# Kernel tuning notes

Hardware: AMD Instinct MI355X
Metric: run time of the kernel (lower is better)

## Reference

```python
import jax, jax.numpy as jnp
import numpy as np

B, L, D, H, DH = 2, 2048, 1024, 16, 64
EPS = 1e-5
ROPE_BASE = 10000.0


def _layernorm(x, w, b):
    mu = jnp.mean(x, axis=-1, keepdims=True)
    var = jnp.var(x, axis=-1, keepdims=True)
    y = (x - mu) * jax.lax.rsqrt(var + EPS)
    y = y * w
    if b is not None:
        y = y + b
    return y


def _rope(x):
    # x: [B, L, H, DH]; GPT-NeoX-style rotation over the full head dim
    inv_freq = 1.0 / (ROPE_BASE ** (jnp.arange(0, DH, 2, dtype=jnp.float32) / DH))  # [DH/2]
    t = jnp.arange(L, dtype=jnp.float32)
    freqs = jnp.outer(t, inv_freq)                       # [L, DH/2]
    cos = jnp.concatenate([jnp.cos(freqs)] * 2, axis=-1)[:, None, :]  # [L, 1, DH]
    sin = jnp.concatenate([jnp.sin(freqs)] * 2, axis=-1)[:, None, :]
    x1, x2 = jnp.split(x, 2, axis=-1)
    rot = jnp.concatenate([-x2, x1], axis=-1)
    return x * cos + rot * sin


def setup_inputs() -> dict:
    key = jax.random.key(0)
    ks = jax.random.split(key, 3)
    x = jax.random.normal(ks[0], (B, L, D), dtype=jnp.float32)
    w_qkv = jax.random.normal(ks[1], (3 * D, D), dtype=jnp.float32) * (D ** -0.5)
    w_out = jax.random.normal(ks[2], (D, D), dtype=jnp.float32) * (D ** -0.5)
    return {
        "x": x,
        "ln_w": jnp.ones((D,), jnp.float32),
        "ln_b": jnp.zeros((D,), jnp.float32),
        "w_qkv": w_qkv,
        "q_ln_w": jnp.ones((D,), jnp.float32),
        "k_ln_w": jnp.ones((D,), jnp.float32),
        "w_out": w_out,
    }


def reference(x, ln_w, ln_b, w_qkv, q_ln_w, k_ln_w, w_out):
    h = _layernorm(x, ln_w, ln_b)                         # [B, L, D]
    qkv = jnp.einsum("bld,ed->ble", h, w_qkv)            # [B, L, 3D]
    q, k, v = jnp.split(qkv, 3, axis=-1)
    q = _layernorm(q, q_ln_w, None)                       # weight-only per-token LN
    k = _layernorm(k, k_ln_w, None)
    q = _rope(q.reshape(B, L, H, DH))                     # [B, L, H, DH]
    k = _rope(k.reshape(B, L, H, DH))
    v = v.reshape(B, L, H, DH)
    ctx = jax.nn.dot_product_attention(q, k, v)           # [B, L, H, DH], scale 1/sqrt(DH)
    ctx = ctx.reshape(B, L, D)
    return jnp.einsum("bld,od->blo", ctx, w_out)
```

## Files before the change

kernel.cpp:

```cpp
#include <hip/hip_runtime.h>
#include <math.h>

#define BB 2
#define LL 2048
#define DD 1024
#define HH 16
#define DHD 64
#define NT (BB*LL)
#define D3 (3*DD)
#define D2 (2*DD)

typedef __bf16 bf16x8 __attribute__((ext_vector_type(8)));
typedef float  f32x4  __attribute__((ext_vector_type(4)));

__device__ __forceinline__ f32x4 mfma16(bf16x8 a, bf16x8 b, f32x4 c) {
    return __builtin_amdgcn_mfma_f32_16x16x32_bf16(a, b, c, 0, 0, 0);
}

__device__ __forceinline__ unsigned short f2bf(float f) {
    unsigned int u = __float_as_uint(f);
    u = (u + 0x7FFFu + ((u >> 16) & 1u)) >> 16;
    return (unsigned short)u;
}
__device__ __forceinline__ float bf2f(unsigned short s) {
    return __uint_as_float(((unsigned int)s) << 16);
}

__device__ __forceinline__ void gload16(const void* g, void* l) {
    __builtin_amdgcn_global_load_lds(
        (const __attribute__((address_space(1))) void*)g,
        (__attribute__((address_space(3))) void*)l, 16, 0, 0);
}

__device__ __forceinline__ float wred(float v) {
#pragma unroll
    for (int off = 32; off > 0; off >>= 1) v += __shfl_down(v, off, 64);
    return v;
}

__device__ __forceinline__ unsigned int pack_bf2(float p0, float p1) {
    const unsigned int u0 = __float_as_uint(p0) + 0x8000u;
    const unsigned int u1 = __float_as_uint(p1) + 0x8000u;
    return __builtin_amdgcn_perm(u1, u0, 0x07060302u);
}

__global__ __launch_bounds__(256) void ln_cvt_kernel(
        const float* __restrict__ x, const float* __restrict__ w,
        const float* __restrict__ b, unsigned short* __restrict__ h,
        const float* __restrict__ wq, unsigned short* __restrict__ wqb,
        const float* __restrict__ wo, unsigned short* __restrict__ wob) {
    const int bx = blockIdx.x;
    const int tid = threadIdx.x;
    if (bx >= NT) {
        int i = (bx - NT) * 256 + tid;
        const float* s; unsigned short* d;
        if (i < 786432) { s = wq; d = wqb; }
        else            { i -= 786432; s = wo; d = wob; }
        const float4 v = ((const float4*)s)[i];
        ((ushort4*)d)[i] = make_ushort4(f2bf(v.x), f2bf(v.y), f2bf(v.z), f2bf(v.w));
        return;
    }
    const float4 v = ((const float4*)(x + (size_t)bx * DD))[tid];
    float s = v.x + v.y + v.z + v.w;
    float ss = v.x*v.x + v.y*v.y + v.z*v.z + v.w*v.w;
    s = wred(s); ss = wred(ss);
    __shared__ float red[8];
    if ((tid & 63) == 0) { red[tid >> 6] = s; red[4 + (tid >> 6)] = ss; }
    __syncthreads();
    s  = red[0] + red[1] + red[2] + red[3];
    ss = red[4] + red[5] + red[6] + red[7];
    const float mu  = s * (1.0f / DD);
    const float inv = rsqrtf(ss * (1.0f / DD) - mu * mu + 1e-5f);
    const float4 wv = ((const float4*)w)[tid];
    const float4 bv = ((const float4*)b)[tid];
    *(ushort4*)(h + (size_t)bx * DD + tid * 4) = make_ushort4(
        f2bf((v.x - mu) * inv * wv.x + bv.x),
        f2bf((v.y - mu) * inv * wv.y + bv.y),
        f2bf((v.z - mu) * inv * wv.z + bv.z),
        f2bf((v.w - mu) * inv * wv.w + bv.w));
}

__global__ __launch_bounds__(256) void gemm_qkv(
        const unsigned short* __restrict__ A, const unsigned short* __restrict__ B,
        unsigned short* __restrict__ qk, unsigned short* __restrict__ vt) {
    const int K = DD;
    __shared__ unsigned short As[128 * 32];
    __shared__ unsigned short Bs[128 * 32];
    const int tid = threadIdx.x;
    const int w = tid >> 6, lane = tid & 63;
    const int l15 = lane & 15, quad = lane >> 4;
    const int wr = w >> 1, wc = w & 1;
    const int m0 = blockIdx.y << 7, n0 = blockIdx.x << 7;

    const int srow = w * 32 + (lane >> 2);
    const int skel = (lane & 3) << 3;
    const unsigned short* gA = A + (size_t)(m0 + srow) * K + skel;
    const unsigned short* gB = B + (size_t)(n0 + srow) * K + skel;
    unsigned short* lA = &As[w * 1024];
    unsigned short* lB = &Bs[w * 1024];

    f32x4 acc[4][4];
#pragma unroll
    for (int i = 0; i < 4; i++)
#pragma unroll
        for (int j = 0; j < 4; j++) acc[i][j] = (f32x4){0.f, 0.f, 0.f, 0.f};

    for (int k0 = 0; k0 < K; k0 += 32) {
        gload16(gA + k0,                 lA);
        gload16(gA + k0 + (size_t)16*K,  lA + 512);
        gload16(gB + k0,                 lB);
        gload16(gB + k0 + (size_t)16*K,  lB + 512);
        __syncthreads();
        bf16x8 af[4], bg[4];
#pragma unroll
        for (int i = 0; i < 4; i++) {
            af[i] = *(const bf16x8*)&As[(wr*64 + i*16 + l15) * 32 + quad*8];
            bg[i] = *(const bf16x8*)&Bs[(wc*64 + i*16 + l15) * 32 + quad*8];
        }
#pragma unroll
        for (int i = 0; i < 4; i++)
#pragma unroll
            for (int j = 0; j < 4; j++)
                acc[i][j] = mfma16(af[i], bg[j], acc[i][j]);
        __syncthreads();
    }
    if (n0 < D2) {
#pragma unroll
        for (int i = 0; i < 4; i++) {
            const int mrow = m0 + wr*64 + i*16 + quad*4;
#pragma unroll
            for (int j = 0; j < 4; j++) {
                const int ncol = n0 + wc*64 + j*16 + l15;
#pragma unroll
                for (int r = 0; r < 4; r++)
                    qk[(size_t)(mrow + r) * D2 + ncol] = f2bf(acc[i][j][r]);
            }
        }
    } else {
#pragma unroll
        for (int i = 0; i < 4; i++) {
            const int mrow = m0 + wr*64 + i*16 + quad*4;
            const int bb = mrow >> 11, l = mrow & (LL - 1);
#pragma unroll
            for (int j = 0; j < 4; j++) {
                const int nv = n0 + wc*64 + j*16 + l15 - D2;
                const int hh = nv >> 6, dh = nv & 63;
                *(ushort4*)&vt[((size_t)(bb*HH + hh) * DHD + dh) * LL + l] =
                    make_ushort4(f2bf(acc[i][j][0]), f2bf(acc[i][j][1]),
                                 f2bf(acc[i][j][2]), f2bf(acc[i][j][3]));
            }
        }
    }
}

__global__ __launch_bounds__(256) void gemm_out(
        const unsigned short* __restrict__ A, const unsigned short* __restrict__ B,
        float* __restrict__ C, int M, int N, int K) {
    __shared__ unsigned short As[128 * 32];
    __shared__ unsigned short Bs[128 * 32];
    const int tid = threadIdx.x;
    const int w = tid >> 6, lane = tid & 63;
    const int l15 = lane & 15, quad = lane >> 4;
    const int wr = w >> 1, wc = w & 1;
    const int m0 = blockIdx.y << 7, n0 = blockIdx.x << 7;
    const int srow = w * 32 + (lane >> 2);
    const int skel = (lane & 3) << 3;
    const unsigned short* gA = A + (size_t)(m0 + srow) * K + skel;
    const unsigned short* gB = B + (size_t)(n0 + srow) * K + skel;
    unsigned short* lA = &As[w * 1024];
    unsigned short* lB = &Bs[w * 1024];
    f32x4 acc[4][4];
#pragma unroll
    for (int i = 0; i < 4; i++)
#pragma unroll
        for (int j = 0; j < 4; j++) acc[i][j] = (f32x4){0.f, 0.f, 0.f, 0.f};
    for (int k0 = 0; k0 < K; k0 += 32) {
        gload16(gA + k0,                 lA);
        gload16(gA + k0 + (size_t)16*K,  lA + 512);
        gload16(gB + k0,                 lB);
        gload16(gB + k0 + (size_t)16*K,  lB + 512);
        __syncthreads();
        bf16x8 af[4], bg[4];
#pragma unroll
        for (int i = 0; i < 4; i++) {
            af[i] = *(const bf16x8*)&As[(wr*64 + i*16 + l15) * 32 + quad*8];
            bg[i] = *(const bf16x8*)&Bs[(wc*64 + i*16 + l15) * 32 + quad*8];
        }
#pragma unroll
        for (int i = 0; i < 4; i++)
#pragma unroll
            for (int j = 0; j < 4; j++)
                acc[i][j] = mfma16(af[i], bg[j], acc[i][j]);
        __syncthreads();
    }
#pragma unroll
    for (int i = 0; i < 4; i++) {
        const int mrow = m0 + wr*64 + i*16 + quad*4;
#pragma unroll
        for (int j = 0; j < 4; j++) {
            const int ncol = n0 + wc*64 + j*16 + l15;
#pragma unroll
            for (int r = 0; r < 4; r++)
                C[(size_t)(mrow + r) * N + ncol] = acc[i][j][r];
        }
    }
}

__global__ __launch_bounds__(256) void qk_rope_kernel(
        const unsigned short* __restrict__ qk,
        const float* __restrict__ qw, const float* __restrict__ kw,
        unsigned short* __restrict__ qarr, unsigned short* __restrict__ karr) {
    const int t = blockIdx.x;
    const int l = t & (LL - 1), b = t >> 11;
    const int tid = threadIdx.x;
    const unsigned short* base = qk + (size_t)t * D2;
    const ushort4 qu = *(const ushort4*)(base + tid * 4);
    const ushort4 ku = *(const ushort4*)(base + DD + tid * 4);
    const float q[4] = {bf2f(qu.x), bf2f(qu.y), bf2f(qu.z), bf2f(qu.w)};
    const float k[4] = {bf2f(ku.x), bf2f(ku.y), bf2f(ku.z), bf2f(ku.w)};
    float sq = q[0]+q[1]+q[2]+q[3], ssq = q[0]*q[0]+q[1]*q[1]+q[2]*q[2]+q[3]*q[3];
    float sk = k[0]+k[1]+k[2]+k[3], ssk = k[0]*k[0]+k[1]*k[1]+k[2]*k[2]+k[3]*k[3];
    sq = wred(sq); ssq = wred(ssq); sk = wred(sk); ssk = wred(ssk);
    __shared__ float red[16];
    __shared__ float qs[DD], ks[DD];
    const int wid = tid >> 6;
    if ((tid & 63) == 0) { red[wid] = sq; red[4+wid] = ssq; red[8+wid] = sk; red[12+wid] = ssk; }
    __syncthreads();
    sq = red[0]+red[1]+red[2]+red[3];    ssq = red[4]+red[5]+red[6]+red[7];
    sk = red[8]+red[9]+red[10]+red[11];  ssk = red[12]+red[13]+red[14]+red[15];
    const float muq = sq * (1.f/DD), invq = rsqrtf(ssq*(1.f/DD) - muq*muq + 1e-5f);
    const float muk = sk * (1.f/DD), invk = rsqrtf(ssk*(1.f/DD) - muk*muk + 1e-5f);
    const float4 qwv = ((const float4*)qw)[tid];
    const float4 kwv = ((const float4*)kw)[tid];
    const float qwa[4] = {qwv.x, qwv.y, qwv.z, qwv.w};
    const float kwa[4] = {kwv.x, kwv.y, kwv.z, kwv.w};
    float qn[4], kn[4];
#pragma unroll
    for (int e = 0; e < 4; e++) {
        qn[e] = (q[e] - muq) * invq * qwa[e];
        kn[e] = (k[e] - muk) * invk * kwa[e];
    }
    *(float4*)&qs[tid*4] = make_float4(qn[0], qn[1], qn[2], qn[3]);
    *(float4*)&ks[tid*4] = make_float4(kn[0], kn[1], kn[2], kn[3]);
    __syncthreads();
    const int d = tid * 4, j0 = d & 63;
    const bool first = (j0 < 32);
    const int pt = first ? (tid + 8) : (tid - 8);
    const float4 qp4 = *(const float4*)&qs[pt*4];
    const float4 kp4 = *(const float4*)&ks[pt*4];
    const float qb[4] = {qp4.x, qp4.y, qp4.z, qp4.w};
    const float kb[4] = {kp4.x, kp4.y, kp4.z, kp4.w};
    const float lf = (float)l;
    const float QS = 0.125f * 1.44269504088896340736f;
    unsigned short oq[4], ok[4];
#pragma unroll
    for (int e = 0; e < 4; e++) {
        const float fi   = (float)((j0 & 31) + e);
        const float freq = expf(fi * (-0.28782313662425576f));
        const float ang  = lf * freq;
        const float c = cosf(ang), sn = sinf(ang);
        float vq, vk;
        if (first) { vq = qn[e]*c - qb[e]*sn; vk = kn[e]*c - kb[e]*sn; }
        else       { vq = qn[e]*c + qb[e]*sn; vk = kn[e]*c + kb[e]*sn; }
        oq[e] = f2bf(vq * QS);
        ok[e] = f2bf(vk);
    }
    const int hh = tid >> 4;
    const int dh = (tid * 4) & 63;
    const size_t ro = ((size_t)(b*HH + hh) * LL + l) * DHD + dh;
    *(ushort4*)(qarr + ro) = make_ushort4(oq[0], oq[1], oq[2], oq[3]);
    *(ushort4*)(karr + ro) = make_ushort4(ok[0], ok[1], ok[2], ok[3]);
}

__global__ __launch_bounds__(256, 4) void attn_kernel(
        const unsigned short* __restrict__ qarr,
        const unsigned short* __restrict__ karr,
        const unsigned short* __restrict__ vt,
        unsigned short* __restrict__ opart,
        float* __restrict__ lpart) {
    const int x = blockIdx.x;
    const int g  = (x & 7) | ((x >> 7) << 3);
    const int qblk = (x >> 3) & 15;
    const int s = g & 1, bh = g >> 1;
    const int b = bh >> 4, h = bh & 15;
    const int q0 = qblk << 7;
    const int kvbase = s << 10;
    const int tid = threadIdx.x, w = tid >> 6, lane = tid & 63;
    const int l15 = lane & 15, quad = lane >> 4;

    __shared__ unsigned short Ks[64 * 64];
    __shared__ unsigned short Vs[64 * 64];
    __shared__ unsigned short Pw[4][2][16][72];

    const unsigned short* kbase = karr + ((size_t)bh * LL + kvbase) * DHD;
    const unsigned short* vbase = vt   + (size_t)bh * DHD * LL + kvbase;

    bf16x8 qf[2][2];
    {
        const unsigned short* qp = qarr + ((size_t)bh*LL + q0 + w*32 + l15) * DHD + quad*8;
#pragma unroll
        for (int qt = 0; qt < 2; qt++)
#pragma unroll
            for (int c = 0; c < 2; c++)
                qf[qt][c] = *(const bf16x8*)(qp + qt*16*DHD + c*32);
    }

    bf16x8 ones;
#pragma unroll
    for (int i = 0; i < 8; i++) ones[i] = (__bf16)1.0f;

    const int r8 = lane >> 3, sc = lane & 7;
    f32x4 o[2][4], lacc[2];
#pragma unroll
    for (int qt = 0; qt < 2; qt++) {
        lacc[qt] = (f32x4){0.f, 0.f, 0.f, 0.f};
#pragma unroll
        for (int nt = 0; nt < 4; nt++) o[qt][nt] = (f32x4){0.f, 0.f, 0.f, 0.f};
    }

#pragma unroll
    for (int rd = 0; rd < 2; rd++) {
        const int row = w*8 + rd*32 + r8;
        const int chunk = sc ^ (row & 7);
        gload16(kbase + (size_t)row * DHD + chunk*8, (char*)Ks + w*1024 + rd*4096);
        gload16(vbase + (size_t)row * LL + chunk*8,  (char*)Vs + w*1024 + rd*4096);
    }

    for (int kt = 0; kt < 16; kt++) {
        __syncthreads();
        bf16x8 kf[4][2], vf[4][2];
#pragma unroll
        for (int t = 0; t < 4; t++)
#pragma unroll
            for (int c = 0; c < 2; c++) {
                const int slot = (quad + c*4) ^ (l15 & 7);
                kf[t][c] = *(const bf16x8*)&Ks[(t*16 + l15) * DHD + slot*8];
                vf[t][c] = *(const bf16x8*)&Vs[(t*16 + l15) * DHD + slot*8];
            }
        __syncthreads();
        if (kt + 1 < 16) {
#pragma unroll
            for (int rd = 0; rd < 2; rd++) {
                const int row = w*8 + rd*32 + r8;
                const int chunk = sc ^ (row & 7);
                gload16(kbase + ((size_t)((kt+1)*64 + row)) * DHD + chunk*8,
                        (char*)Ks + w*1024 + rd*4096);
                gload16(vbase + (size_t)row * LL + (kt+1)*64 + chunk*8,
                        (char*)Vs + w*1024 + rd*4096);
            }
        }

#pragma unroll
        for (int qt = 0; qt < 2; qt++) {
            f32x4 st[4];
#pragma unroll
            for (int t = 0; t < 4; t++) {
                f32x4 z = (f32x4){-64.f, -64.f, -64.f, -64.f};
                z = mfma16(kf[t][0], qf[qt][0], z);
                z = mfma16(kf[t][1], qf[qt][1], z);
                st[t] = z;
            }
#pragma unroll
            for (int t = 0; t < 4; t++) {
                const float p0 = __builtin_amdgcn_exp2f(st[t][0]);
                const float p1 = __builtin_amdgcn_exp2f(st[t][1]);
                const float p2 = __builtin_amdgcn_exp2f(st[t][2]);
                const float p3 = __builtin_amdgcn_exp2f(st[t][3]);
                uint2 pk;
                pk.x = pack_bf2(p0, p1);
                pk.y = pack_bf2(p2, p3);
                *(uint2*)&Pw[w][qt][l15][t*16 + quad*4] = pk;
            }
            const bf16x8 ap0 = *(const bf16x8*)&Pw[w][qt][l15][quad*8];
            const bf16x8 ap1 = *(const bf16x8*)&Pw[w][qt][l15][32 + quad*8];
            lacc[qt] = mfma16(ap0, ones, lacc[qt]);
            lacc[qt] = mfma16(ap1, ones, lacc[qt]);
#pragma unroll
            for (int nt = 0; nt < 4; nt++) {
                f32x4 t0 = o[qt][nt];
                t0 = mfma16(ap0, vf[nt][0], t0);
                t0 = mfma16(ap1, vf[nt][1], t0);
                o[qt][nt] = t0;
            }
        }
    }

    unsigned short* op = opart + (size_t)s * NT * DD;
#pragma unroll
    for (int qt = 0; qt < 2; qt++) {
#pragma unroll
        for (int r = 0; r < 4; r++) {
            const int qrow = q0 + w*32 + qt*16 + quad*4 + r;
            const size_t token = (size_t)b * LL + qrow;
#pragma unroll
            for (int nt = 0; nt < 4; nt++)
                op[token * DD + h*DHD + nt*16 + l15] = f2bf(o[qt][nt][r]);
        }
        if (l15 == 0) {
#pragma unroll
            for (int r = 0; r < 4; r++)
                lpart[((size_t)s * BB*HH + bh) * LL + q0 + w*32 + qt*16 + quad*4 + r] =
                    lacc[qt][r];
        }
    }
}

__global__ __launch_bounds__(256) void combine_kernel(
        const unsigned short* __restrict__ opart, const float* __restrict__ lpart,
        unsigned short* __restrict__ ctx) {
    const int token = blockIdx.x;
    const int tid = threadIdx.x;
    const int b = token >> 11, l = token & (LL - 1);
    const int h = tid >> 4;
    const size_t idx = (size_t)token * DD + tid * 4;
    const ushort4 a = *(const ushort4*)(opart + idx);
    const ushort4 c = *(const ushort4*)(opart + (size_t)NT * DD + idx);
    const float l1 = lpart[((size_t)(b*HH + h)) * LL + l];
    const float l2 = lpart[((size_t)BB*HH*LL) + ((size_t)(b*HH + h)) * LL + l];
    const float inv = 1.0f / (l1 + l2);
    *(ushort4*)(ctx + idx) = make_ushort4(
        f2bf((bf2f(a.x) + bf2f(c.x)) * inv),
        f2bf((bf2f(a.y) + bf2f(c.y)) * inv),
        f2bf((bf2f(a.z) + bf2f(c.z)) * inv),
        f2bf((bf2f(a.w) + bf2f(c.w)) * inv));
}

extern "C" void kernel_launch(void* const* d_in, const int* in_sizes, int n_in,
                              void* d_out, int out_size, void* d_ws, size_t ws_size,
                              hipStream_t stream) {
    const float* x      = (const float*)d_in[0];
    const float* ln_w   = (const float*)d_in[1];
    const float* ln_b   = (const float*)d_in[2];
    const float* w_qkv  = (const float*)d_in[3];
    const float* q_ln_w = (const float*)d_in[4];
    const float* k_ln_w = (const float*)d_in[5];
    const float* w_out  = (const float*)d_in[6];
    float* out = (float*)d_out;

    char* ws = (char*)d_ws;
    unsigned short* hb    = (unsigned short*)ws;
    unsigned short* karr  = (unsigned short*)ws;
    unsigned short* ctxb  = (unsigned short*)ws;
    unsigned short* qk    = (unsigned short*)(ws + ((size_t)8  << 20));
    unsigned short* opart = (unsigned short*)(ws + ((size_t)8  << 20));
    unsigned short* vtp   = (unsigned short*)(ws + ((size_t)24 << 20));
    unsigned short* qarr  = (unsigned short*)(ws + ((size_t)32 << 20));
    unsigned short* wqb   = (unsigned short*)(ws + ((size_t)40 << 20));
    float*          lpart = (float*)(ws + ((size_t)40 << 20));
    unsigned short* wob   = (unsigned short*)(ws + ((size_t)46 << 20));

    ln_cvt_kernel<<<NT + 4096, 256, 0, stream>>>(x, ln_w, ln_b, hb,
                                                 w_qkv, wqb, w_out, wob);
    gemm_qkv<<<dim3(D3/128, NT/128), 256, 0, stream>>>(hb, wqb, qk, vtp);
    qk_rope_kernel<<<NT, 256, 0, stream>>>(qk, q_ln_w, k_ln_w, qarr, karr);
    attn_kernel<<<1024, 256, 0, stream>>>(qarr, karr, vtp, opart, lpart);
    combine_kernel<<<NT, 256, 0, stream>>>(opart, lpart, ctxb);
    gemm_out<<<dim3(DD/128, NT/128), 256, 0, stream>>>(ctxb, wob, out, NT, DD, DD);
}
```

Baseline: 245.8 us.

## Split attention KV into four chunks and halve output GEMM row tile

```diff
diff --git a/kernel.cpp b/kernel.cpp
--- a/kernel.cpp
+++ b/kernel.cpp
@@ -9,6 +9,8 @@
 #define NT (BB*LL)
 #define D3 (3*DD)
 #define D2 (2*DD)
+#define NSPLIT 4
+#define KVCH (LL/NSPLIT)
 
 typedef __bf16 bf16x8 __attribute__((ext_vector_type(8)));
 typedef float  f32x4  __attribute__((ext_vector_type(4)));
@@ -156,46 +158,45 @@
 __global__ __launch_bounds__(256) void gemm_out(
         const unsigned short* __restrict__ A, const unsigned short* __restrict__ B,
         float* __restrict__ C, int M, int N, int K) {
-    __shared__ unsigned short As[128 * 32];
+    __shared__ unsigned short As[64 * 32];
     __shared__ unsigned short Bs[128 * 32];
     const int tid = threadIdx.x;
     const int w = tid >> 6, lane = tid & 63;
     const int l15 = lane & 15, quad = lane >> 4;
     const int wr = w >> 1, wc = w & 1;
-    const int m0 = blockIdx.y << 7, n0 = blockIdx.x << 7;
-    const int srow = w * 32 + (lane >> 2);
+    const int m0 = blockIdx.y << 6, n0 = blockIdx.x << 7;
     const int skel = (lane & 3) << 3;
-    const unsigned short* gA = A + (size_t)(m0 + srow) * K + skel;
-    const unsigned short* gB = B + (size_t)(n0 + srow) * K + skel;
-    unsigned short* lA = &As[w * 1024];
+    const unsigned short* gA = A + (size_t)(m0 + w*16 + (lane >> 2)) * K + skel;
+    const unsigned short* gB = B + (size_t)(n0 + w*32 + (lane >> 2)) * K + skel;
+    unsigned short* lA = &As[w * 512];
     unsigned short* lB = &Bs[w * 1024];
-    f32x4 acc[4][4];
-#pragma unroll
-    for (int i = 0; i < 4; i++)
+    f32x4 acc[2][4];
+#pragma unroll
+    for (int i = 0; i < 2; i++)
 #pragma unroll
         for (int j = 0; j < 4; j++) acc[i][j] = (f32x4){0.f, 0.f, 0.f, 0.f};
     for (int k0 = 0; k0 < K; k0 += 32) {
         gload16(gA + k0,                 lA);
-        gload16(gA + k0 + (size_t)16*K,  lA + 512);
         gload16(gB + k0,                 lB);
         gload16(gB + k0 + (size_t)16*K,  lB + 512);
         __syncthreads();
-        bf16x8 af[4], bg[4];
-#pragma unroll
-        for (int i = 0; i < 4; i++) {
-            af[i] = *(const bf16x8*)&As[(wr*64 + i*16 + l15) * 32 + quad*8];
-            bg[i] = *(const bf16x8*)&Bs[(wc*64 + i*16 + l15) * 32 + quad*8];
-        }
-#pragma unroll
-        for (int i = 0; i < 4; i++)
+        bf16x8 af[2], bg[4];
+#pragma unroll
+        for (int i = 0; i < 2; i++)
+            af[i] = *(const bf16x8*)&As[(wr*32 + i*16 + l15) * 32 + quad*8];
+#pragma unroll
+        for (int j = 0; j < 4; j++)
+            bg[j] = *(const bf16x8*)&Bs[(wc*64 + j*16 + l15) * 32 + quad*8];
+#pragma unroll
+        for (int i = 0; i < 2; i++)
 #pragma unroll
             for (int j = 0; j < 4; j++)
                 acc[i][j] = mfma16(af[i], bg[j], acc[i][j]);
         __syncthreads();
     }
 #pragma unroll
-    for (int i = 0; i < 4; i++) {
-        const int mrow = m0 + wr*64 + i*16 + quad*4;
+    for (int i = 0; i < 2; i++) {
+        const int mrow = m0 + wr*32 + i*16 + quad*4;
 #pragma unroll
         for (int j = 0; j < 4; j++) {
             const int ncol = n0 + wc*64 + j*16 + l15;
@@ -276,21 +277,22 @@
         const unsigned short* __restrict__ qarr,
         const unsigned short* __restrict__ karr,
         const unsigned short* __restrict__ vt,
-        unsigned short* __restrict__ opart,
+        unsigned short* __restrict__ op0, unsigned short* __restrict__ op1,
+        unsigned short* __restrict__ op2, unsigned short* __restrict__ op3,
         float* __restrict__ lpart) {
     const int x = blockIdx.x;
     const int g  = (x & 7) | ((x >> 7) << 3);
     const int qblk = (x >> 3) & 15;
-    const int s = g & 1, bh = g >> 1;
+    const int s = g & 3, bh = g >> 2;
     const int b = bh >> 4, h = bh & 15;
     const int q0 = qblk << 7;
-    const int kvbase = s << 10;
+    const int kvbase = s * KVCH;
     const int tid = threadIdx.x, w = tid >> 6, lane = tid & 63;
     const int l15 = lane & 15, quad = lane >> 4;
 
     __shared__ unsigned short Ks[64 * 64];
     __shared__ unsigned short Vs[64 * 64];
-    __shared__ unsigned short Pw[4][2][16][72];
+    __shared__ unsigned short Pw[4][16][72];
 
     const unsigned short* kbase = karr + ((size_t)bh * LL + kvbase) * DHD;
     const unsigned short* vbase = vt   + (size_t)bh * DHD * LL + kvbase;
@@ -326,7 +328,7 @@
         gload16(vbase + (size_t)row * LL + chunk*8,  (char*)Vs + w*1024 + rd*4096);
     }
 
-    for (int kt = 0; kt < 16; kt++) {
+    for (int kt = 0; kt < KVCH/64; kt++) {
         __syncthreads();
         bf16x8 kf[4][2], vf[4][2];
 #pragma unroll
@@ -338,7 +340,7 @@
                 vf[t][c] = *(const bf16x8*)&Vs[(t*16 + l15) * DHD + slot*8];
             }
         __syncthreads();
-        if (kt + 1 < 16) {
+        if (kt + 1 < KVCH/64) {
 #pragma unroll
             for (int rd = 0; rd < 2; rd++) {
                 const int row = w*8 + rd*32 + r8;
@@ -369,10 +371,10 @@
                 uint2 pk;
                 pk.x = pack_bf2(p0, p1);
                 pk.y = pack_bf2(p2, p3);
-                *(uint2*)&Pw[w][qt][l15][t*16 + quad*4] = pk;
-            }
-            const bf16x8 ap0 = *(const bf16x8*)&Pw[w][qt][l15][quad*8];
-            const bf16x8 ap1 = *(const bf16x8*)&Pw[w][qt][l15][32 + quad*8];
+                *(uint2*)&Pw[w][l15][t*16 + quad*4] = pk;
+            }
+            const bf16x8 ap0 = *(const bf16x8*)&Pw[w][l15][quad*8];
+            const bf16x8 ap1 = *(const bf16x8*)&Pw[w][l15][32 + quad*8];
             lacc[qt] = mfma16(ap0, ones, lacc[qt]);
             lacc[qt] = mfma16(ap1, ones, lacc[qt]);
 #pragma unroll
@@ -385,7 +387,7 @@
         }
     }
 
-    unsigned short* op = opart + (size_t)s * NT * DD;
+    unsigned short* op = (s == 0) ? op0 : (s == 1) ? op1 : (s == 2) ? op2 : op3;
 #pragma unroll
     for (int qt = 0; qt < 2; qt++) {
 #pragma unroll
@@ -406,23 +408,27 @@
 }
 
 __global__ __launch_bounds__(256) void combine_kernel(
-        const unsigned short* __restrict__ opart, const float* __restrict__ lpart,
-        unsigned short* __restrict__ ctx) {
+        const unsigned short* __restrict__ op0, const unsigned short* __restrict__ op1,
+        const unsigned short* __restrict__ op2, const unsigned short* __restrict__ op3,
+        const float* __restrict__ lpart, unsigned short* __restrict__ ctx) {
     const int token = blockIdx.x;
     const int tid = threadIdx.x;
     const int b = token >> 11, l = token & (LL - 1);
     const int h = tid >> 4;
     const size_t idx = (size_t)token * DD + tid * 4;
-    const ushort4 a = *(const ushort4*)(opart + idx);
-    const ushort4 c = *(const ushort4*)(opart + (size_t)NT * DD + idx);
-    const float l1 = lpart[((size_t)(b*HH + h)) * LL + l];
-    const float l2 = lpart[((size_t)BB*HH*LL) + ((size_t)(b*HH + h)) * LL + l];
-    const float inv = 1.0f / (l1 + l2);
+    const ushort4 a0 = *(const ushort4*)(op0 + idx);
+    const ushort4 a1 = *(const ushort4*)(op1 + idx);
+    const ushort4 a2 = *(const ushort4*)(op2 + idx);
+    const ushort4 a3 = *(const ushort4*)(op3 + idx);
+    const size_t lbase = (size_t)(b*HH + h) * LL + l;
+    const float lsum = lpart[lbase] + lpart[(size_t)BB*HH*LL + lbase]
+                     + lpart[2*(size_t)BB*HH*LL + lbase] + lpart[3*(size_t)BB*HH*LL + lbase];
+    const float inv = 1.0f / lsum;
     *(ushort4*)(ctx + idx) = make_ushort4(
-        f2bf((bf2f(a.x) + bf2f(c.x)) * inv),
-        f2bf((bf2f(a.y) + bf2f(c.y)) * inv),
-        f2bf((bf2f(a.z) + bf2f(c.z)) * inv),
-        f2bf((bf2f(a.w) + bf2f(c.w)) * inv));
+        f2bf((bf2f(a0.x) + bf2f(a1.x) + bf2f(a2.x) + bf2f(a3.x)) * inv),
+        f2bf((bf2f(a0.y) + bf2f(a1.y) + bf2f(a2.y) + bf2f(a3.y)) * inv),
+        f2bf((bf2f(a0.z) + bf2f(a1.z) + bf2f(a2.z) + bf2f(a3.z)) * inv),
+        f2bf((bf2f(a0.w) + bf2f(a1.w) + bf2f(a2.w) + bf2f(a3.w)) * inv));
 }
 
 extern "C" void kernel_launch(void* const* d_in, const int* in_sizes, int n_in,
@@ -440,20 +446,23 @@
     char* ws = (char*)d_ws;
     unsigned short* hb    = (unsigned short*)ws;
     unsigned short* karr  = (unsigned short*)ws;
-    unsigned short* ctxb  = (unsigned short*)ws;
     unsigned short* qk    = (unsigned short*)(ws + ((size_t)8  << 20));
-    unsigned short* opart = (unsigned short*)(ws + ((size_t)8  << 20));
+    unsigned short* op0   = (unsigned short*)(ws + ((size_t)8  << 20));
+    unsigned short* op1   = (unsigned short*)(ws + ((size_t)16 << 20));
     unsigned short* vtp   = (unsigned short*)(ws + ((size_t)24 << 20));
     unsigned short* qarr  = (unsigned short*)(ws + ((size_t)32 << 20));
-    unsigned short* wqb   = (unsigned short*)(ws + ((size_t)40 << 20));
-    float*          lpart = (float*)(ws + ((size_t)40 << 20));
-    unsigned short* wob   = (unsigned short*)(ws + ((size_t)46 << 20));
+    unsigned short* ctxb  = (unsigned short*)(ws + ((size_t)32 << 20));
+    unsigned short* op2   = (unsigned short*)(ws + ((size_t)40 << 20));
+    unsigned short* op3   = (unsigned short*)(ws + ((size_t)48 << 20));
+    unsigned short* wqb   = (unsigned short*)(ws + ((size_t)56 << 20));
+    float*          lpart = (float*)(ws + ((size_t)56 << 20));
+    unsigned short* wob   = (unsigned short*)(ws + ((size_t)62 << 20));
 
     ln_cvt_kernel<<<NT + 4096, 256, 0, stream>>>(x, ln_w, ln_b, hb,
                                                  w_qkv, wqb, w_out, wob);
     gemm_qkv<<<dim3(D3/128, NT/128), 256, 0, stream>>>(hb, wqb, qk, vtp);
     qk_rope_kernel<<<NT, 256, 0, stream>>>(qk, q_ln_w, k_ln_w, qarr, karr);
-    attn_kernel<<<1024, 256, 0, stream>>>(qarr, karr, vtp, opart, lpart);
-    combine_kernel<<<NT, 256, 0, stream>>>(opart, lpart, ctxb);
-    gemm_out<<<dim3(DD/128, NT/128), 256, 0, stream>>>(ctxb, wob, out, NT, DD, DD);
-}
+    attn_kernel<<<2048, 256, 0, stream>>>(qarr, karr, vtp, op0, op1, op2, op3, lpart);
+    combine_kernel<<<NT, 256, 0, stream>>>(op0, op1, op2, op3, lpart, ctxb);
+    gemm_out<<<dim3(DD/128, NT/64), 256, 0, stream>>>(ctxb, wob, out, NT, DD, DD);
+}
```

New measurement: 278.8 us. 1.13x slower.
